# Kernel tuning notes

Measured on AMD Instinct MI355X. Metric: run time of the kernel, lower is better.

Reference implementation:

```python
import jax, jax.numpy as jnp
import numpy as np


def conv1d(x, w, b, pad):
    # x: (B, Cin, T), w: (Cout, Cin, K), b: (Cout,)
    y = jax.lax.conv_general_dilated(x, w, window_strides=(1,), padding=[(pad, pad)],
                                     dimension_numbers=('NCH', 'OIH', 'NCH'))
    return y + b[None, :, None]


def setup_inputs() -> dict:
    key = jax.random.key(0)
    ks = jax.random.split(key, 16)
    B, Cmel, Ctxt, Catt, T1, T2 = 16, 80, 256, 80, 800, 200
    s = 0.05
    return {
        'queries': jax.random.normal(ks[0], (B, Cmel, T1), jnp.float32),
        'keys': jax.random.normal(ks[1], (B, Ctxt, T2), jnp.float32),
        'attn_prior': jax.random.uniform(ks[2], (B, T1, T2), jnp.float32),
        # key_proj: Conv1d(256->512,k=3,pad=1) -> ReLU -> Conv1d(512->80,k=1)
        'kw1': jax.random.normal(ks[3], (Ctxt * 2, Ctxt, 3), jnp.float32) * s,
        'kb1': jax.random.normal(ks[4], (Ctxt * 2,), jnp.float32) * s,
        'kw2': jax.random.normal(ks[5], (Catt, Ctxt * 2, 1), jnp.float32) * s,
        'kb2': jax.random.normal(ks[6], (Catt,), jnp.float32) * s,
        # query_proj (3xconv): 80->160 k3 -> ReLU -> 160->80 k1 -> ReLU -> 80->80 k1
        'qw1': jax.random.normal(ks[7], (Cmel * 2, Cmel, 3), jnp.float32) * s,
        'qb1': jax.random.normal(ks[8], (Cmel * 2,), jnp.float32) * s,
        'qw2': jax.random.normal(ks[9], (Cmel, Cmel * 2, 1), jnp.float32) * s,
        'qb2': jax.random.normal(ks[10], (Cmel,), jnp.float32) * s,
        'qw3': jax.random.normal(ks[11], (Catt, Cmel, 1), jnp.float32) * s,
        'qb3': jax.random.normal(ks[12], (Catt,), jnp.float32) * s,
    }


def reference(queries, keys, attn_prior, kw1, kb1, kw2, kb2, qw1, qb1, qw2, qb2, qw3, qb3):
    # key encoder
    k = jax.nn.relu(conv1d(keys, kw1, kb1, pad=1))
    k = conv1d(k, kw2, kb2, pad=0)                      # (B, Catt, T2)
    # query encoder ('3xconv')
    q = jax.nn.relu(conv1d(queries, qw1, qb1, pad=1))
    q = jax.nn.relu(conv1d(q, qw2, qb2, pad=0))
    q = conv1d(q, qw3, qb3, pad=0)                      # (B, Catt, T1)
    # L2 distance over channels: ||q||^2 + ||k||^2 - 2 q.k (same math as broadcast (q-k)^2 sum)
    q2 = jnp.sum(q * q, axis=1)                         # (B, T1)
    k2 = jnp.sum(k * k, axis=1)                         # (B, T2)
    qk = jnp.einsum('bct,bcs->bts', q, k)               # (B, T1, T2)
    attn = -0.0005 * (q2[:, :, None] + k2[:, None, :] - 2.0 * qk)[:, None]  # (B,1,T1,T2)
    attn = jax.nn.log_softmax(attn, axis=3) + jnp.log(attn_prior[:, None] + 1e-8)
    return attn
```

## Files before the change

### kernel.cpp

```cpp
#include <hip/hip_runtime.h>
#include <cstdint>
#include <cmath>

using short8  = __attribute__((ext_vector_type(8))) short;
using short4v = __attribute__((ext_vector_type(4))) short;
using floatx4 = __attribute__((ext_vector_type(4))) float;

__device__ __forceinline__ short f2bf(float f) {
  union { float f; unsigned u; } x; x.f = f;
  unsigned r = x.u + 0x7FFFu + ((x.u >> 16) & 1u);
  return (short)(r >> 16);
}

__global__ __launch_bounds__(256) void prep_kernel(
    const float* __restrict__ keys, const float* __restrict__ queries,
    const float* __restrict__ kw1, const float* __restrict__ kw2,
    const float* __restrict__ qw1, const float* __restrict__ qw2,
    const float* __restrict__ qw3,
    short* __restrict__ kT0, short* __restrict__ qT0,
    short* __restrict__ w1, short* __restrict__ w2, short* __restrict__ w3,
    short* __restrict__ w4, short* __restrict__ w5)
{
  const int bid = blockIdx.x, tid = threadIdx.x;
  __shared__ float xs[32][65];

  if (bid < 1136) {
    const float* src; short* dst; int CIN, T, CP, bx, by, b;
    if (bid < 512) {
      src = keys; dst = kT0; CIN = 256; T = 200; CP = 256;
      bx = bid & 3; by = (bid >> 2) & 7; b = bid >> 5;
    } else {
      int b2 = bid - 512;
      src = queries; dst = qT0; CIN = 80; T = 800; CP = 96;
      bx = b2 % 13; by = (b2 / 13) % 3; b = b2 / 39;
    }
    const int t0 = bx * 64, ci0 = by * 32;
    for (int i = tid; i < 32 * 64; i += 256) {
      int row = i >> 6, col = i & 63;
      float v = 0.f;
      if (ci0 + row < CIN && t0 + col < T)
        v = src[((size_t)b * CIN + ci0 + row) * T + t0 + col];
      xs[row][col] = v;
    }
    __syncthreads();
    int t = tid >> 2, c8 = (tid & 3) * 8;
    if (t0 + t < T) {
      short8 o;
      #pragma unroll
      for (int j = 0; j < 8; ++j) o[j] = f2bf(xs[c8 + j][t]);
      *(short8*)&dst[((size_t)b * T + t0 + t) * CP + ci0 + c8] = o;
    }
  } else {
    int blk = bid - 1136;
    const float* src; short* dst; int base;
    int CoP, CiP, Cout, CIN, K;
    if      (blk < 384) { src=kw1; dst=w1; base=0;   CoP=512; CiP=256; Cout=512; CIN=256; K=3; }
    else if (blk < 432) { src=kw2; dst=w2; base=384; CoP=96;  CiP=512; Cout=80;  CIN=512; K=1; }
    else if (blk < 486) { src=qw1; dst=w3; base=432; CoP=192; CiP=96;  Cout=160; CIN=80;  K=3; }
    else if (blk < 504) { src=qw2; dst=w4; base=486; CoP=96;  CiP=192; Cout=80;  CIN=160; K=1; }
    else                { src=qw3; dst=w5; base=504; CoP=96;  CiP=96;  Cout=80;  CIN=80;  K=1; }
    int tot = K * CoP * CiP;
    int b0 = (blk - base) * 1024;
    for (int e = 0; e < 4; ++e) {
      int gi = b0 + e * 256 + tid;
      if (gi < tot) {
        int dk  = gi / (CoP * CiP);
        int rem = gi - dk * (CoP * CiP);
        int co  = rem / CiP, ci = rem - (rem / CiP) * CiP;
        float v = (co < Cout && ci < CIN) ? src[((size_t)co * CIN + ci) * K + dk] : 0.f;
        dst[gi] = f2bf(v);
      }
    }
  }
}

__global__ __launch_bounds__(256) void conv_k3_kernel(
    const short* __restrict__ kT0, const short* __restrict__ qT0,
    const short* __restrict__ w1, const short* __restrict__ w3,
    const short* __restrict__ w4, const short* __restrict__ w5,
    const float* __restrict__ kb1, const float* __restrict__ qb1,
    const float* __restrict__ qb2, const float* __restrict__ qb3,
    short* __restrict__ kT1, short* __restrict__ qF)
{
  __shared__ __align__(16) short smem[25680];
  const int tid = threadIdx.x, wid = tid >> 6, lane = tid & 63;
  const int q = lane >> 4, m = lane & 15;
  short* xs = smem;

  if (blockIdx.x < 512) {
    const int blk = blockIdx.x;
    const int b = blk >> 5, co0 = ((blk >> 2) & 7) * 64, t0 = (blk & 3) * 64;
    const int wy = wid >> 1, wx = wid & 1;
    short* as = smem + 2640;

    floatx4 acc[2][2];
    #pragma unroll
    for (int i = 0; i < 2; ++i)
      #pragma unroll
      for (int j = 0; j < 2; ++j) acc[i][j] = (floatx4){0.f, 0.f, 0.f, 0.f};

    for (int c0 = 0; c0 < 8; ++c0) {
      __syncthreads();
      for (int i = tid; i < 66 * 4; i += 256) {
        int row = i >> 2, c8 = (i & 3) * 8;
        int t = t0 + row - 1;
        int4 v = {0, 0, 0, 0};
        if (t >= 0 && t < 200)
          v = *(const int4*)&kT0[((size_t)b * 200 + t) * 256 + c0 * 32 + c8];
        *(int4*)&xs[row * 40 + c8] = v;
      }
      for (int i = tid; i < 192 * 4; i += 256) {
        int row = i >> 2, c8 = (i & 3) * 8;
        int dk = row >> 6, co = row & 63;
        *(int4*)&as[row * 40 + c8] =
            *(const int4*)&w1[((size_t)(dk * 512 + co0 + co)) * 256 + c0 * 32 + c8];
      }
      __syncthreads();
      #pragma unroll
      for (int dk = 0; dk < 3; ++dk) {
        short8 fa0 = *(const short8*)&as[(dk * 64 + wy * 32 + m) * 40 + q * 8];
        short8 fa1 = *(const short8*)&as[(dk * 64 + wy * 32 + 16 + m) * 40 + q * 8];
        #pragma unroll
        for (int j = 0; j < 2; ++j) {
          short8 fb = *(const short8*)&xs[(wx * 32 + j * 16 + m + dk) * 40 + q * 8];
          acc[0][j] = __builtin_amdgcn_mfma_f32_16x16x32_bf16(fa0, fb, acc[0][j], 0, 0, 0);
          acc[1][j] = __builtin_amdgcn_mfma_f32_16x16x32_bf16(fa1, fb, acc[1][j], 0, 0, 0);
        }
      }
    }
    #pragma unroll
    for (int i = 0; i < 2; ++i) {
      #pragma unroll
      for (int j = 0; j < 2; ++j) {
        #pragma unroll
        for (int r = 0; r < 4; ++r) {
          int co = co0 + wy * 32 + i * 16 + q * 4 + r;
          int t  = t0 + wx * 32 + j * 16 + m;
          if (t < 200) {
            float v = fmaxf(acc[i][j][r] + kb1[co], 0.f);
            kT1[((size_t)b * 200 + t) * 512 + co] = f2bf(v);
          }
        }
      }
    }
  } else {
    const int qbid = blockIdx.x - 512;
    const int b = qbid / 13, t0 = (qbid % 13) * 64;
    short* y1c = smem + 2640;
    short* y2c = smem + 18000;

    floatx4 accq[3][4];
    #pragma unroll
    for (int f = 0; f < 3; ++f)
      #pragma unroll
      for (int tf = 0; tf < 4; ++tf) accq[f][tf] = (floatx4){0.f, 0.f, 0.f, 0.f};

    for (int c0 = 0; c0 < 3; ++c0) {
      __syncthreads();
      for (int i = tid; i < 66 * 4; i += 256) {
        int row = i >> 2, c8 = (i & 3) * 8;
        int t = t0 + row - 1;
        int4 v = {0, 0, 0, 0};
        if (t >= 0 && t < 800)
          v = *(const int4*)&qT0[((size_t)b * 800 + t) * 96 + c0 * 32 + c8];
        *(int4*)&xs[row * 40 + c8] = v;
      }
      __syncthreads();
      #pragma unroll
      for (int dk = 0; dk < 3; ++dk) {
        short8 fa[3];
        #pragma unroll
        for (int f = 0; f < 3; ++f)
          fa[f] = *(const short8*)&w3[((size_t)(dk * 192 + wid * 48 + f * 16 + m)) * 96
                                      + c0 * 32 + q * 8];
        #pragma unroll
        for (int tf = 0; tf < 4; ++tf) {
          short8 fb = *(const short8*)&xs[(tf * 16 + m + dk) * 40 + q * 8];
          #pragma unroll
          for (int f = 0; f < 3; ++f)
            accq[f][tf] = __builtin_amdgcn_mfma_f32_16x16x32_bf16(fa[f], fb, accq[f][tf], 0, 0, 0);
        }
      }
    }
    __syncthreads();
    #pragma unroll
    for (int f = 0; f < 3; ++f) {
      #pragma unroll
      for (int tf = 0; tf < 4; ++tf) {
        int co = wid * 48 + f * 16 + q * 4;
        int t  = tf * 16 + m;
        short4v o;
        #pragma unroll
        for (int r = 0; r < 4; ++r) {
          float bv = (co + r < 160) ? qb1[co + r] : 0.f;
          o[r] = f2bf(fmaxf(accq[f][tf][r] + bv, 0.f));
        }
        *(short4v*)&y1c[(co >> 5) * 2560 + t * 40 + (co & 31)] = o;
      }
    }
    __syncthreads();

    floatx4 acc2q[6];
    #pragma unroll
    for (int f = 0; f < 6; ++f) acc2q[f] = (floatx4){0.f, 0.f, 0.f, 0.f};
    #pragma unroll
    for (int c = 0; c < 6; ++c) {
      short8 fb = *(const short8*)&y1c[c * 2560 + (wid * 16 + m) * 40 + q * 8];
      #pragma unroll
      for (int f = 0; f < 6; ++f) {
        short8 fa = *(const short8*)&w4[((size_t)(f * 16 + m)) * 192 + c * 32 + q * 8];
        acc2q[f] = __builtin_amdgcn_mfma_f32_16x16x32_bf16(fa, fb, acc2q[f], 0, 0, 0);
      }
    }
    #pragma unroll
    for (int f = 0; f < 6; ++f) {
      int co = f * 16 + q * 4;
      int t  = wid * 16 + m;
      short4v o;
      #pragma unroll
      for (int r = 0; r < 4; ++r) {
        float bv = (co + r < 80) ? qb2[co + r] : 0.f;
        o[r] = f2bf(fmaxf(acc2q[f][r] + bv, 0.f));
      }
      *(short4v*)&y2c[(co >> 5) * 2560 + t * 40 + (co & 31)] = o;
    }
    __syncthreads();

    floatx4 acc3q[6];
    #pragma unroll
    for (int f = 0; f < 6; ++f) acc3q[f] = (floatx4){0.f, 0.f, 0.f, 0.f};
    #pragma unroll
    for (int c = 0; c < 3; ++c) {
      short8 fb = *(const short8*)&y2c[c * 2560 + (wid * 16 + m) * 40 + q * 8];
      #pragma unroll
      for (int f = 0; f < 6; ++f) {
        short8 fa = *(const short8*)&w5[((size_t)(f * 16 + m)) * 96 + c * 32 + q * 8];
        acc3q[f] = __builtin_amdgcn_mfma_f32_16x16x32_bf16(fa, fb, acc3q[f], 0, 0, 0);
      }
    }
    int t = t0 + wid * 16 + m;
    if (t < 800) {
      #pragma unroll
      for (int f = 0; f < 6; ++f) {
        int co = f * 16 + q * 4;
        short4v o;
        #pragma unroll
        for (int r = 0; r < 4; ++r) {
          float bv = (co + r < 80) ? qb3[co + r] : 0.f;
          o[r] = f2bf(acc3q[f][r] + bv);
        }
        *(short4v*)&qF[((size_t)b * 800 + t) * 96 + co] = o;
      }
    }
  }
}

__global__ __launch_bounds__(64) void kconv2_kernel(
    const short* __restrict__ kT1, const short* __restrict__ w2,
    const float* __restrict__ kb2, short* __restrict__ kF)
{
  const int blk = blockIdx.x;
  const int b = blk / 13, t0 = (blk - b * 13) * 16;
  const int lane = threadIdx.x & 63;
  const int q = lane >> 4, m = lane & 15;
  const int t = t0 + m;
  const bool tv = (t < 200);

  floatx4 acc[6];
  #pragma unroll
  for (int f = 0; f < 6; ++f) acc[f] = (floatx4){0.f, 0.f, 0.f, 0.f};

  #pragma unroll
  for (int c = 0; c < 16; ++c) {
    short8 fb;
    if (tv) fb = *(const short8*)&kT1[((size_t)b * 200 + t) * 512 + c * 32 + q * 8];
    else    fb = (short8){0,0,0,0,0,0,0,0};
    #pragma unroll
    for (int f = 0; f < 6; ++f) {
      short8 fa = *(const short8*)&w2[((size_t)(f * 16 + m)) * 512 + c * 32 + q * 8];
      acc[f] = __builtin_amdgcn_mfma_f32_16x16x32_bf16(fa, fb, acc[f], 0, 0, 0);
    }
  }
  if (tv) {
    #pragma unroll
    for (int f = 0; f < 6; ++f) {
      int co = f * 16 + q * 4;
      short4v o;
      #pragma unroll
      for (int r = 0; r < 4; ++r) {
        float bv = (co + r < 80) ? kb2[co + r] : 0.f;
        o[r] = f2bf(acc[f][r] + bv);
      }
      *(short4v*)&kF[((size_t)b * 200 + t) * 96 + co] = o;
    }
  }
}

__global__ __launch_bounds__(256) void attn_mfma(
    const short* __restrict__ qT, const short* __restrict__ kT,
    const float* __restrict__ prior, float* __restrict__ out)
{
  const int b = blockIdx.y, t1_0 = blockIdx.x * 64;
  const int tid = threadIdx.x, wid = tid >> 6, lane = tid & 63;
  const int q = lane >> 4, m = lane & 15;

  __shared__ __align__(16) char smem[51200];
  short* aq = (short*)smem;
  short* bk = (short*)(smem + 13312);
  float* k2s = (float*)(smem + 29952);
  float* sstage = (float*)smem;

  floatx4 acc[13];
  #pragma unroll
  for (int f = 0; f < 13; ++f) acc[f] = (floatx4){0.f, 0.f, 0.f, 0.f};

  for (int i = tid; i < 64 * 12; i += 256) {
    int row = i / 12, g = i - (i / 12) * 12;
    int4 v = {0, 0, 0, 0};
    if (t1_0 + row < 800)
      v = *(const int4*)&qT[((size_t)b * 800 + t1_0 + row) * 96 + g * 8];
    *(int4*)&aq[row * 104 + g * 8] = v;
  }

  float k2acc = 0.f;
  for (int c = 0; c < 3; ++c) {
    __syncthreads();
    for (int i = tid; i < 208 * 4; i += 256) {
      int row = i >> 2, g = i & 3;
      int4 v = {0, 0, 0, 0};
      if (row < 200)
        v = *(const int4*)&kT[((size_t)b * 200 + row) * 96 + c * 32 + g * 8];
      *(int4*)&bk[row * 40 + g * 8] = v;
    }
    __syncthreads();
    if (tid < 208) {
      #pragma unroll
      for (int g = 0; g < 4; ++g) {
        short8 s = *(const short8*)&bk[tid * 40 + g * 8];
        #pragma unroll
        for (int j = 0; j < 8; ++j) {
          union { unsigned u; float f; } x; x.u = ((unsigned)(unsigned short)s[j]) << 16;
          k2acc = fmaf(x.f, x.f, k2acc);
        }
      }
    }
    short8 fa = *(const short8*)&aq[(wid * 16 + m) * 104 + c * 32 + q * 8];
    #pragma unroll
    for (int f = 0; f < 13; ++f) {
      short8 fb = *(const short8*)&bk[(f * 16 + m) * 40 + q * 8];
      acc[f] = __builtin_amdgcn_mfma_f32_16x16x32_bf16(fa, fb, acc[f], 0, 0, 0);
    }
  }
  if (tid < 208) k2s[tid] = k2acc;
  __syncthreads();

  float k2v[13];
  #pragma unroll
  for (int f = 0; f < 13; ++f) k2v[f] = k2s[f * 16 + m];

  float mx[4] = {-INFINITY, -INFINITY, -INFINITY, -INFINITY};
  #pragma unroll
  for (int f = 0; f < 13; ++f) {
    bool valid = (f * 16 + m) < 200;
    #pragma unroll
    for (int r = 0; r < 4; ++r) {
      float v = valid ? (0.001f * acc[f][r] - 0.0005f * k2v[f]) : -INFINITY;
      acc[f][r] = v;
      mx[r] = fmaxf(mx[r], v);
    }
  }
  #pragma unroll
  for (int msk = 1; msk < 16; msk <<= 1)
    #pragma unroll
    for (int r = 0; r < 4; ++r) mx[r] = fmaxf(mx[r], __shfl_xor(mx[r], msk));
  float sm[4] = {0.f, 0.f, 0.f, 0.f};
  #pragma unroll
  for (int f = 0; f < 13; ++f)
    #pragma unroll
    for (int r = 0; r < 4; ++r) sm[r] += __expf(acc[f][r] - mx[r]);
  #pragma unroll
  for (int msk = 1; msk < 16; msk <<= 1)
    #pragma unroll
    for (int r = 0; r < 4; ++r) sm[r] += __shfl_xor(sm[r], msk);
  float lse[4];
  #pragma unroll
  for (int r = 0; r < 4; ++r) lse[r] = mx[r] + __logf(sm[r]);

  __syncthreads();
  #pragma unroll
  for (int f = 0; f < 13; ++f) {
    int col = f * 16 + m;
    if (col < 200) {
      #pragma unroll
      for (int r = 0; r < 4; ++r)
        sstage[(wid * 16 + q * 4 + r) * 200 + col] = acc[f][r] - lse[r];
    }
  }
  __syncthreads();

  for (int i = tid; i < 64 * 50; i += 256) {
    int row = i / 50, seg = i - (i / 50) * 50;
    int t1 = t1_0 + row;
    if (t1 < 800) {
      size_t o = ((size_t)b * 800 + t1) * 200 + seg * 4;
      floatx4 pv = *(const floatx4*)&prior[o];
      floatx4 sv = *(const floatx4*)&sstage[row * 200 + seg * 4];
      floatx4 ov;
      #pragma unroll
      for (int j = 0; j < 4; ++j) ov[j] = sv[j] + __logf(pv[j] + 1e-8f);
      *(floatx4*)&out[o] = ov;
    }
  }
}

extern "C" void kernel_launch(void* const* d_in, const int* in_sizes, int n_in,
                              void* d_out, int out_size, void* d_ws, size_t ws_size,
                              hipStream_t stream) {
  const float* queries = (const float*)d_in[0];
  const float* keys    = (const float*)d_in[1];
  const float* prior   = (const float*)d_in[2];
  const float* kw1 = (const float*)d_in[3];
  const float* kb1 = (const float*)d_in[4];
  const float* kw2 = (const float*)d_in[5];
  const float* kb2 = (const float*)d_in[6];
  const float* qw1 = (const float*)d_in[7];
  const float* qb1 = (const float*)d_in[8];
  const float* qw2 = (const float*)d_in[9];
  const float* qb2 = (const float*)d_in[10];
  const float* qw3 = (const float*)d_in[11];
  const float* qb3 = (const float*)d_in[12];
  float* out = (float*)d_out;

  short* p = (short*)d_ws;
  short* kT0 = p;  p += (size_t)3200 * 256;
  short* qT0 = p;  p += (size_t)12800 * 96;
  short* w1  = p;  p += (size_t)3 * 512 * 256;
  short* w2  = p;  p += (size_t)96 * 512;
  short* w3  = p;  p += (size_t)3 * 192 * 96;
  short* w4  = p;  p += (size_t)96 * 192;
  short* w5  = p;  p += (size_t)96 * 96;
  short* kT1 = p;  p += (size_t)3200 * 512;
  short* kF  = p;  p += (size_t)3200 * 96;
  short* qF  = p;  p += (size_t)12800 * 96;

  prep_kernel<<<dim3(1649), 256, 0, stream>>>(keys, queries, kw1, kw2, qw1, qw2, qw3,
                                              kT0, qT0, w1, w2, w3, w4, w5);
  conv_k3_kernel<<<dim3(720), 256, 0, stream>>>(kT0, qT0, w1, w3, w4, w5,
                                                kb1, qb1, qb2, qb3, kT1, qF);
  kconv2_kernel<<<dim3(208), 64, 0, stream>>>(kT1, w2, kb2, kF);
  attn_mfma<<<dim3(13, 16), 256, 0, stream>>>(qF, kF, prior, out);
}
```

Before: 139.3 us.

## Double-buffer key conv weights via direct global-to-LDS loads, preload full input tiles

```diff
diff --git a/kernel.cpp b/kernel.cpp
--- a/kernel.cpp
+++ b/kernel.cpp
@@ -10,6 +10,12 @@
   union { float f; unsigned u; } x; x.f = f;
   unsigned r = x.u + 0x7FFFu + ((x.u >> 16) & 1u);
   return (short)(r >> 16);
+}
+
+__device__ __forceinline__ void gl_lds16(const short* g, short* l) {
+  __builtin_amdgcn_global_load_lds(
+      (const __attribute__((address_space(1))) void*)g,
+      (__attribute__((address_space(3))) void*)l, 16, 0, 0);
 }
 
 __global__ __launch_bounds__(256) void prep_kernel(
@@ -53,8 +59,8 @@
   } else {
     int blk = bid - 1136;
     const float* src; short* dst; int base;
-    int CoP, CiP, Cout, CIN, K;
-    if      (blk < 384) { src=kw1; dst=w1; base=0;   CoP=512; CiP=256; Cout=512; CIN=256; K=3; }
+    int CoP, CiP, Cout, CIN, K; bool isW1 = false;
+    if      (blk < 384) { src=kw1; dst=w1; base=0;   CoP=512; CiP=256; Cout=512; CIN=256; K=3; isW1=true; }
     else if (blk < 432) { src=kw2; dst=w2; base=384; CoP=96;  CiP=512; Cout=80;  CIN=512; K=1; }
     else if (blk < 486) { src=qw1; dst=w3; base=432; CoP=192; CiP=96;  Cout=160; CIN=80;  K=3; }
     else if (blk < 504) { src=qw2; dst=w4; base=486; CoP=96;  CiP=192; Cout=80;  CIN=160; K=1; }
@@ -68,7 +74,9 @@
         int rem = gi - dk * (CoP * CiP);
         int co  = rem / CiP, ci = rem - (rem / CiP) * CiP;
         float v = (co < Cout && ci < CIN) ? src[((size_t)co * CIN + ci) * K + dk] : 0.f;
-        dst[gi] = f2bf(v);
+        int idx = gi;
+        if (isW1) idx = (((ci >> 5) * 3 + dk) * 512 + co) * 32 + (ci & 31);
+        dst[idx] = f2bf(v);
       }
     }
   }
@@ -82,16 +90,17 @@
     const float* __restrict__ qb2, const float* __restrict__ qb3,
     short* __restrict__ kT1, short* __restrict__ qF)
 {
-  __shared__ __align__(16) short smem[25680];
+  __shared__ __align__(16) short smem[29904];
   const int tid = threadIdx.x, wid = tid >> 6, lane = tid & 63;
   const int q = lane >> 4, m = lane & 15;
-  short* xs = smem;
 
   if (blockIdx.x < 512) {
     const int blk = blockIdx.x;
     const int b = blk >> 5, co0 = ((blk >> 2) & 7) * 64, t0 = (blk & 3) * 64;
     const int wy = wid >> 1, wx = wid & 1;
-    short* as = smem + 2640;
+    short* xs = smem;
+    short* asb0 = smem + 17424;
+    short* asb1 = smem + 23568;
 
     floatx4 acc[2][2];
     #pragma unroll
@@ -99,34 +108,50 @@
       #pragma unroll
       for (int j = 0; j < 2; ++j) acc[i][j] = (floatx4){0.f, 0.f, 0.f, 0.f};
 
+    for (int i = tid; i < 66 * 32; i += 256) {
+      int row = i >> 5, c8 = (i & 31) * 8;
+      int t = t0 + row - 1;
+      int4 v = {0, 0, 0, 0};
+      if (t >= 0 && t < 200)
+        v = *(const int4*)&kT0[((size_t)b * 200 + t) * 256 + c8];
+      *(int4*)&xs[row * 264 + c8] = v;
+    }
+    {
+      const int wv = tid >> 6;
+      #pragma unroll
+      for (int c = 0; c < 3; ++c) {
+        const short* g = w1 + ((size_t)(0 * 3 + c) * 512 + co0) * 32 + tid * 8;
+        short* l = asb0 + c * 2048 + wv * 512;
+        gl_lds16(g, l);
+      }
+    }
+    __syncthreads();
+
+    int cur = 0;
     for (int c0 = 0; c0 < 8; ++c0) {
-      __syncthreads();
-      for (int i = tid; i < 66 * 4; i += 256) {
-        int row = i >> 2, c8 = (i & 3) * 8;
-        int t = t0 + row - 1;
-        int4 v = {0, 0, 0, 0};
-        if (t >= 0 && t < 200)
-          v = *(const int4*)&kT0[((size_t)b * 200 + t) * 256 + c0 * 32 + c8];
-        *(int4*)&xs[row * 40 + c8] = v;
-      }
-      for (int i = tid; i < 192 * 4; i += 256) {
-        int row = i >> 2, c8 = (i & 3) * 8;
-        int dk = row >> 6, co = row & 63;
-        *(int4*)&as[row * 40 + c8] =
-            *(const int4*)&w1[((size_t)(dk * 512 + co0 + co)) * 256 + c0 * 32 + c8];
-      }
-      __syncthreads();
+      short* as_cur = cur ? asb1 : asb0;
+      if (c0 < 7) {
+        short* asn = cur ? asb0 : asb1;
+        const int wv = tid >> 6;
+        #pragma unroll
+        for (int c = 0; c < 3; ++c) {
+          const short* g = w1 + ((size_t)((c0 + 1) * 3 + c) * 512 + co0) * 32 + tid * 8;
+          gl_lds16(g, asn + c * 2048 + wv * 512);
+        }
+      }
       #pragma unroll
       for (int dk = 0; dk < 3; ++dk) {
-        short8 fa0 = *(const short8*)&as[(dk * 64 + wy * 32 + m) * 40 + q * 8];
-        short8 fa1 = *(const short8*)&as[(dk * 64 + wy * 32 + 16 + m) * 40 + q * 8];
+        short8 fa0 = *(const short8*)&as_cur[dk * 2048 + (wy * 32 + m) * 32 + q * 8];
+        short8 fa1 = *(const short8*)&as_cur[dk * 2048 + (wy * 32 + 16 + m) * 32 + q * 8];
         #pragma unroll
         for (int j = 0; j < 2; ++j) {
-          short8 fb = *(const short8*)&xs[(wx * 32 + j * 16 + m + dk) * 40 + q * 8];
+          short8 fb = *(const short8*)&xs[(wx * 32 + j * 16 + m + dk) * 264 + c0 * 32 + q * 8];
           acc[0][j] = __builtin_amdgcn_mfma_f32_16x16x32_bf16(fa0, fb, acc[0][j], 0, 0, 0);
           acc[1][j] = __builtin_amdgcn_mfma_f32_16x16x32_bf16(fa1, fb, acc[1][j], 0, 0, 0);
         }
       }
+      __syncthreads();
+      cur ^= 1;
     }
     #pragma unroll
     for (int i = 0; i < 2; ++i) {
@@ -146,8 +171,9 @@
   } else {
     const int qbid = blockIdx.x - 512;
     const int b = qbid / 13, t0 = (qbid % 13) * 64;
-    short* y1c = smem + 2640;
-    short* y2c = smem + 18000;
+    short* xs2 = smem;
+    short* y1c = smem + 6864;
+    short* y2c = smem + 22224;
 
     floatx4 accq[3][4];
     #pragma unroll
@@ -155,17 +181,17 @@
       #pragma unroll
       for (int tf = 0; tf < 4; ++tf) accq[f][tf] = (floatx4){0.f, 0.f, 0.f, 0.f};
 
+    for (int i = tid; i < 66 * 12; i += 256) {
+      int row = i / 12, g = i - (i / 12) * 12;
+      int t = t0 + row - 1;
+      int4 v = {0, 0, 0, 0};
+      if (t >= 0 && t < 800)
+        v = *(const int4*)&qT0[((size_t)b * 800 + t) * 96 + g * 8];
+      *(int4*)&xs2[row * 104 + g * 8] = v;
+    }
+    __syncthreads();
+
     for (int c0 = 0; c0 < 3; ++c0) {
-      __syncthreads();
-      for (int i = tid; i < 66 * 4; i += 256) {
-        int row = i >> 2, c8 = (i & 3) * 8;
-        int t = t0 + row - 1;
-        int4 v = {0, 0, 0, 0};
-        if (t >= 0 && t < 800)
-          v = *(const int4*)&qT0[((size_t)b * 800 + t) * 96 + c0 * 32 + c8];
-        *(int4*)&xs[row * 40 + c8] = v;
-      }
-      __syncthreads();
       #pragma unroll
       for (int dk = 0; dk < 3; ++dk) {
         short8 fa[3];
@@ -175,7 +201,7 @@
                                       + c0 * 32 + q * 8];
         #pragma unroll
         for (int tf = 0; tf < 4; ++tf) {
-          short8 fb = *(const short8*)&xs[(tf * 16 + m + dk) * 40 + q * 8];
+          short8 fb = *(const short8*)&xs2[(tf * 16 + m + dk) * 104 + c0 * 32 + q * 8];
           #pragma unroll
           for (int f = 0; f < 3; ++f)
             accq[f][tf] = __builtin_amdgcn_mfma_f32_16x16x32_bf16(fa[f], fb, accq[f][tf], 0, 0, 0);
```

After: 146.8 us. 5.3% more time.
